# Kernel tuning notes

Measured on AMD Instinct MI355X. Metric: run time of the kernel, lower is better.

## Reference

```python
import jax, jax.numpy as jnp
import numpy as np

B, IN, H, NH = 8192, 1024, 2048, 4
HD = H // NH
EPS = 1e-5


def setup_inputs() -> dict:
    key = jax.random.key(0)
    ks = jax.random.split(key, 8)
    s = 0.02
    return {
        "h_prev": jax.random.normal(ks[0], (B, 1, H), jnp.float32),
        "x": jax.random.normal(ks[1], (B, IN), jnp.float32),
        "W_proj": jax.random.normal(ks[2], (H, IN), jnp.float32) * s,
        "b_proj": jnp.zeros((H,), jnp.float32),
        "W_q": jax.random.normal(ks[3], (H, H), jnp.float32) * s,
        "b_q": jnp.zeros((H,), jnp.float32),
        "W_o": jax.random.normal(ks[4], (H, H), jnp.float32) * s,
        "b_o": jnp.zeros((H,), jnp.float32),
        "W_g": jax.random.normal(ks[5], (H, 2 * H), jnp.float32) * s,
        "b_g": jnp.zeros((H,), jnp.float32),
        "gamma": jnp.ones((H,), jnp.float32),
        "beta": jnp.zeros((H,), jnp.float32),
    }


def _layernorm(y, gamma, beta):
    mu = jnp.mean(y, axis=-1, keepdims=True)
    var = jnp.mean(jnp.square(y - mu), axis=-1, keepdims=True)
    return (y - mu) * jax.lax.rsqrt(var + EPS) * gamma + beta


def reference(h_prev, x, W_proj, b_proj, W_q, b_q, W_o, b_o, W_g, b_g, gamma, beta):
    # input projection: [B, IN] -> [B, H]
    x_proj = x @ W_proj.T + b_proj
    x_exp = x_proj[:, None, :]                      # [B, 1, H]
    # 4-element context along seq dim: [B, 4, H]
    context = jnp.concatenate([h_prev, x_exp, h_prev + x_exp, h_prev * x_exp], axis=1)
    # attention with q_len=1, kv_len=4
    q = (h_prev @ W_q.T + b_q).reshape(B, 1, NH, HD).transpose(0, 2, 1, 3)   # [B,NH,1,HD]
    k = context.reshape(B, 4, NH, HD).transpose(0, 2, 1, 3)                   # [B,NH,4,HD]
    scores = jnp.einsum('bhqd,bhkd->bhqk', q, k) / jnp.sqrt(jnp.float32(HD))  # [B,NH,1,4]
    w = jax.nn.softmax(scores, axis=-1)
    attn = jnp.einsum('bhqk,bhkd->bhqd', w, k)                                # v = k
    attn = attn.transpose(0, 2, 1, 3).reshape(B, 1, H)
    attn = attn @ W_o.T + b_o
    attn = jax.nn.gelu(attn, approximate=False)     # torch F.gelu default is exact erf
    gate_in = jnp.concatenate([h_prev, attn], axis=-1)  # [B,1,2H]
    gate = jax.nn.sigmoid(gate_in @ W_g.T + b_g)
    h_cand = _layernorm(attn + h_prev, gamma, beta)
    h_new = gate * h_cand + (1.0 - gate) * h_prev
    return h_new
```

## Files before the change

### kernel.cpp

```cpp
#include <hip/hip_runtime.h>
#include <hip/hip_bf16.h>
#include <math.h>

#define BATCH 8192
#define IN_DIM 1024
#define H_DIM 2048
#define NHEAD 4
#define HEAD_DIM 512
#define EPS_LN 1e-5f

#define BM 256
#define BN 256
#define BKQ 32
#define NBUF 4

typedef __bf16 bf16x8 __attribute__((ext_vector_type(8)));
typedef short s16x8 __attribute__((ext_vector_type(8)));
typedef float f32x4 __attribute__((ext_vector_type(4)));

__device__ __forceinline__ float b2f(short s) {
  union { unsigned u; float f; } v;
  v.u = ((unsigned)(unsigned short)s) << 16;
  return v.f;
}
__device__ __forceinline__ short f2b(float f) {
  union { float f; unsigned u; } v;
  v.f = f;
  unsigned r = v.u + 0x7fffu + ((v.u >> 16) & 1u);
  return (short)(r >> 16);
}

__device__ __forceinline__ void async_ld16(const short* g, const short* l) {
  __builtin_amdgcn_global_load_lds(
      (const __attribute__((address_space(1))) void*)g,
      (__attribute__((address_space(3))) void*)l, 16, 0, 0);
}

__global__ __launch_bounds__(256) void cvt_k(const float* __restrict__ s,
                                             short* __restrict__ d, int n) {
  int i = (blockIdx.x * 256 + threadIdx.x) * 8;
  if (i >= n) return;
  f32x4 a = *(const f32x4*)(s + i);
  f32x4 b = *(const f32x4*)(s + i + 4);
  s16x8 o;
#pragma unroll
  for (int j = 0; j < 4; j++) o[j] = f2b(a[j]);
#pragma unroll
  for (int j = 0; j < 4; j++) o[4 + j] = f2b(b[j]);
  *(s16x8*)(d + i) = o;
}

enum { EPI_BIAS = 0, EPI_GELU = 1, EPI_GATE = 2 };

template <bool DUAL>
__device__ __forceinline__ void stage_tile(
    const short* __restrict__ A, const short* __restrict__ A2,
    const short* __restrict__ W, short* __restrict__ lds, int t, int K,
    int lda, int rowBase, int colBase, int wv, int rsub, int swz) {
  const int k0 = t * BKQ;
  const short* Asrc = A;
  int ak = k0;
  if (DUAL && k0 >= H_DIM) { Asrc = A2; ak = k0 - H_DIM; }
  short* As = lds + (t & (NBUF - 1)) * (BM * BKQ);
  short* Bs = lds + NBUF * BM * BKQ + (t & (NBUF - 1)) * (BN * BKQ);
  const int r0 = wv * 32;
#pragma unroll
  for (int c = 0; c < 2; c++) {
    const int ra = r0 + c * 16 + rsub;
    async_ld16(Asrc + (size_t)(rowBase + ra) * lda + ak + swz,
               As + (r0 + c * 16) * BKQ);
    async_ld16(W + (size_t)(colBase + ra) * K + k0 + swz,
               Bs + (r0 + c * 16) * BKQ);
  }
}

template <int EPI, bool DUAL>
__global__ __launch_bounds__(512, 2) void gemm_bt(
    const short* __restrict__ A, const short* __restrict__ A2,
    const short* __restrict__ W, const float* __restrict__ bias,
    void* __restrict__ Cv, int K, int lda,
    const short* __restrict__ attg, const float* __restrict__ hprev,
    const float* __restrict__ mu, const float* __restrict__ rstd,
    const float* __restrict__ gamma, const float* __restrict__ beta) {
  extern __shared__ __attribute__((aligned(16))) short lds[];
  const int tid = threadIdx.x;
  const int wv = tid >> 6;
  const int lane = tid & 63;
  const int f = blockIdx.y * gridDim.x + blockIdx.x;
  const int ty = f & 7;
  const int tx = f >> 3;
  const int rowBase = tx * BM;
  const int colBase = ty * BN;
  const int wm = wv >> 2;
  const int wn = wv & 3;
  const int fr = lane & 15;
  const int rsub = lane >> 2;
  const int swz = ((lane & 3) ^ ((lane >> 2) & 3)) << 3;
  const int cbt = ((lane >> 4) ^ (lane & 3)) << 3;
  const int NT = K / BKQ;

  f32x4 acc[8][4] = {};

  stage_tile<DUAL>(A, A2, W, lds, 0, K, lda, rowBase, colBase, wv, rsub, swz);
  stage_tile<DUAL>(A, A2, W, lds, 1, K, lda, rowBase, colBase, wv, rsub, swz);
  stage_tile<DUAL>(A, A2, W, lds, 2, K, lda, rowBase, colBase, wv, rsub, swz);
  asm volatile("s_waitcnt vmcnt(8)" ::: "memory");
  __builtin_amdgcn_s_barrier();
  asm volatile("" ::: "memory");

  for (int t = 0; t < NT; ++t) {
    if (t + 3 < NT)
      stage_tile<DUAL>(A, A2, W, lds, t + 3, K, lda, rowBase, colBase, wv,
                       rsub, swz);

    const short* As = lds + (t & (NBUF - 1)) * (BM * BKQ);
    const short* Bs = lds + NBUF * BM * BKQ + (t & (NBUF - 1)) * (BN * BKQ);
    bf16x8 af[8], bfr[4];
    const short* ap = As + (wm * 128 + fr) * BKQ + cbt;
#pragma unroll
    for (int mi = 0; mi < 8; mi++)
      af[mi] = *(const bf16x8*)(ap + mi * (16 * BKQ));
    const short* bp = Bs + (wn * 64 + fr) * BKQ + cbt;
#pragma unroll
    for (int ni = 0; ni < 4; ni++)
      bfr[ni] = *(const bf16x8*)(bp + ni * (16 * BKQ));

    __builtin_amdgcn_s_setprio(1);
#pragma unroll
    for (int mi = 0; mi < 8; mi++)
#pragma unroll
      for (int ni = 0; ni < 4; ni++)
        acc[mi][ni] = __builtin_amdgcn_mfma_f32_16x16x32_bf16(
            af[mi], bfr[ni], acc[mi][ni], 0, 0, 0);
    __builtin_amdgcn_s_setprio(0);

    if (t + 1 < NT) {
      if (t + 3 < NT)
        asm volatile("s_waitcnt vmcnt(8) lgkmcnt(0)" ::: "memory");
      else if (t + 2 < NT)
        asm volatile("s_waitcnt vmcnt(4) lgkmcnt(0)" ::: "memory");
      else
        asm volatile("s_waitcnt vmcnt(0) lgkmcnt(0)" ::: "memory");
      __builtin_amdgcn_s_barrier();
      asm volatile("" ::: "memory");
    }
  }

  const int ocol0 = colBase + wn * 64 + fr;
  const int orow0 = rowBase + wm * 128 + ((lane >> 4) << 2);
#pragma unroll
  for (int mi = 0; mi < 8; mi++) {
#pragma unroll
    for (int ni = 0; ni < 4; ni++) {
      const int col = ocol0 + ni * 16;
      const float bia = bias[col];
#pragma unroll
      for (int r = 0; r < 4; r++) {
        const int row = orow0 + mi * 16 + r;
        float v = acc[mi][ni][r] + bia;
        const size_t idx = (size_t)row * H_DIM + col;
        if (EPI == EPI_BIAS) {
          ((short*)Cv)[idx] = f2b(v);
        } else if (EPI == EPI_GELU) {
          float g = 0.5f * v * (1.0f + erff(v * 0.70710678118654752f));
          ((short*)Cv)[idx] = f2b(g);
        } else {
          float gate = 1.0f / (1.0f + expf(-v));
          float hp = hprev[idx];
          float y = hp + b2f(attg[idx]);
          float hc = (y - mu[row]) * rstd[row] * gamma[col] + beta[col];
          ((float*)Cv)[idx] = gate * hc + (1.0f - gate) * hp;
        }
      }
    }
  }
}

__global__ __launch_bounds__(256) void attn_k(short* __restrict__ qa,
                                              const float* __restrict__ h,
                                              const short* __restrict__ xp) {
  const int lane = threadIdx.x & 63;
  const int pair = blockIdx.x * 4 + (threadIdx.x >> 6);
  const size_t base =
      (size_t)(pair >> 2) * H_DIM + (size_t)(pair & 3) * HEAD_DIM + lane * 8;
  s16x8 qv = *(const s16x8*)(qa + base);
  f32x4 h0 = *(const f32x4*)(h + base);
  f32x4 h1 = *(const f32x4*)(h + base + 4);
  s16x8 xv = *(const s16x8*)(xp + base);
  float hf[8], xf[8];
  float s1 = 0.f, s2 = 0.f, s4 = 0.f;
#pragma unroll
  for (int j = 0; j < 8; j++) {
    float qf = b2f(qv[j]);
    hf[j] = (j < 4) ? h0[j] : h1[j - 4];
    xf[j] = b2f(xv[j]);
    s1 += qf * hf[j];
    s2 += qf * xf[j];
    s4 += qf * hf[j] * xf[j];
  }
#pragma unroll
  for (int off = 32; off > 0; off >>= 1) {
    s1 += __shfl_xor(s1, off, 64);
    s2 += __shfl_xor(s2, off, 64);
    s4 += __shfl_xor(s4, off, 64);
  }
  const float scale = 0.04419417382415922f;
  float t1 = s1 * scale, t2 = s2 * scale, t3 = (s1 + s2) * scale, t4 = s4 * scale;
  float mx = fmaxf(fmaxf(t1, t2), fmaxf(t3, t4));
  float e1 = expf(t1 - mx), e2 = expf(t2 - mx), e3 = expf(t3 - mx), e4 = expf(t4 - mx);
  float inv = 1.0f / (e1 + e2 + e3 + e4);
  float w1 = e1 * inv, w2 = e2 * inv, w3 = e3 * inv, w4 = e4 * inv;
  float ch = w1 + w3, cx = w2 + w3;
  s16x8 o;
#pragma unroll
  for (int j = 0; j < 8; j++)
    o[j] = f2b(ch * hf[j] + cx * xf[j] + w4 * hf[j] * xf[j]);
  *(s16x8*)(qa + base) = o;
}

__global__ __launch_bounds__(256) void rowstats_k(
    const short* __restrict__ attg, const float* __restrict__ h,
    float* __restrict__ mu, float* __restrict__ rstd) {
  __shared__ float sm[8];
  const int row = blockIdx.x;
  const int tid = threadIdx.x;
  const size_t base = (size_t)row * H_DIM + tid * 8;
  s16x8 a = *(const s16x8*)(attg + base);
  f32x4 h0 = *(const f32x4*)(h + base);
  f32x4 h1 = *(const f32x4*)(h + base + 4);
  float s = 0.f, ss = 0.f;
#pragma unroll
  for (int j = 0; j < 8; j++) {
    float y = b2f(a[j]) + ((j < 4) ? h0[j] : h1[j - 4]);
    s += y;
    ss += y * y;
  }
#pragma unroll
  for (int off = 32; off > 0; off >>= 1) {
    s += __shfl_xor(s, off, 64);
    ss += __shfl_xor(ss, off, 64);
  }
  if ((tid & 63) == 0) {
    sm[tid >> 6] = s;
    sm[4 + (tid >> 6)] = ss;
  }
  __syncthreads();
  if (tid == 0) {
    float S = sm[0] + sm[1] + sm[2] + sm[3];
    float SS = sm[4] + sm[5] + sm[6] + sm[7];
    float m = S * (1.0f / H_DIM);
    float var = SS * (1.0f / H_DIM) - m * m;
    mu[row] = m;
    rstd[row] = rsqrtf(fmaxf(var, 0.0f) + EPS_LN);
  }
}

extern "C" void kernel_launch(void* const* d_in, const int* in_sizes, int n_in,
                              void* d_out, int out_size, void* d_ws,
                              size_t ws_size, hipStream_t stream) {
  (void)in_sizes; (void)n_in; (void)out_size; (void)ws_size;
  const float* h_prev = (const float*)d_in[0];
  const float* x      = (const float*)d_in[1];
  const float* W_proj = (const float*)d_in[2];
  const float* b_proj = (const float*)d_in[3];
  const float* W_q    = (const float*)d_in[4];
  const float* b_q    = (const float*)d_in[5];
  const float* W_o    = (const float*)d_in[6];
  const float* b_o    = (const float*)d_in[7];
  const float* W_g    = (const float*)d_in[8];
  const float* b_g    = (const float*)d_in[9];
  const float* gamma  = (const float*)d_in[10];
  const float* beta   = (const float*)d_in[11];
  float* out = (float*)d_out;

  const size_t BH = (size_t)BATCH * H_DIM;
  const size_t BI = (size_t)BATCH * IN_DIM;
  const size_t NWP = (size_t)H_DIM * IN_DIM;
  const size_t NWQ = (size_t)H_DIM * H_DIM;
  const size_t NWG = (size_t)H_DIM * 2 * H_DIM;

  short* h_bf = (short*)d_ws;
  short* x_bf = h_bf + BH;
  short* wp   = x_bf + BI;
  short* wq   = wp + NWP;
  short* wo   = wq + NWQ;
  short* wg   = wo + NWQ;
  short* bufA = wg + NWG;
  short* bufB = bufA + BH;
  float* mu   = (float*)(bufB + BH);
  float* rstd = mu + BATCH;

  dim3 blk(512);
  dim3 grd(BATCH / BM, H_DIM / BN);
  const int SMEM = 2 * NBUF * BM * BKQ * (int)sizeof(short);
  (void)hipFuncSetAttribute((const void*)gemm_bt<EPI_BIAS, false>,
                            hipFuncAttributeMaxDynamicSharedMemorySize, SMEM);
  (void)hipFuncSetAttribute((const void*)gemm_bt<EPI_GELU, false>,
                            hipFuncAttributeMaxDynamicSharedMemorySize, SMEM);
  (void)hipFuncSetAttribute((const void*)gemm_bt<EPI_GATE, true>,
                            hipFuncAttributeMaxDynamicSharedMemorySize, SMEM);

  dim3 cblk(256);
#define CVT(src, dst, n) \
  cvt_k<<<dim3(((n) / 8 + 255) / 256), cblk, 0, stream>>>(src, dst, (int)(n))

  CVT(h_prev, h_bf, BH);
  CVT(x, x_bf, BI);
  CVT(W_proj, wp, NWP);
  CVT(W_q, wq, NWQ);
  CVT(W_o, wo, NWQ);
  CVT(W_g, wg, NWG);
#undef CVT

  gemm_bt<EPI_BIAS, false><<<grd, blk, SMEM, stream>>>(
      x_bf, nullptr, wp, b_proj, bufA, IN_DIM, IN_DIM,
      nullptr, nullptr, nullptr, nullptr, nullptr, nullptr);
  gemm_bt<EPI_BIAS, false><<<grd, blk, SMEM, stream>>>(
      h_bf, nullptr, wq, b_q, bufB, H_DIM, H_DIM,
      nullptr, nullptr, nullptr, nullptr, nullptr, nullptr);
  attn_k<<<dim3(BATCH * NHEAD / 4), cblk, 0, stream>>>(bufB, h_prev, bufA);
  gemm_bt<EPI_GELU, false><<<grd, blk, SMEM, stream>>>(
      bufB, nullptr, wo, b_o, bufA, H_DIM, H_DIM,
      nullptr, nullptr, nullptr, nullptr, nullptr, nullptr);
  rowstats_k<<<dim3(BATCH), cblk, 0, stream>>>(bufA, h_prev, mu, rstd);
  gemm_bt<EPI_GATE, true><<<grd, blk, SMEM, stream>>>(
      h_bf, bufA, wg, b_g, out, 2 * H_DIM, H_DIM,
      bufA, h_prev, mu, rstd, gamma, beta);
}
```

Baseline: 615.4 us.

## Switch GEMM to BK=64 double-buffered pipeline with mid-tile prefetch issue

Replaces the 4-stage BK=32 LDS ring with a 2-stage BK=64 double buffer. Each k-tile is split into two MFMA halves, and the next-next tile's global loads are issued between them after a barrier. Also changes the LDS XOR swizzle to an 8-chunk scheme and drops the grouped block-index remapping in favour of the plain grid order. The aim is fewer barriers per K and better overlap of loads with MFMA work. The cost is a shallower prefetch distance, an extra barrier per tile, and possibly worse L2 locality from the unremapped grid.

```diff
diff --git a/kernel.cpp b/kernel.cpp
--- a/kernel.cpp
+++ b/kernel.cpp
@@ -11,8 +11,7 @@
 
 #define BM 256
 #define BN 256
-#define BKQ 32
-#define NBUF 4
+#define BK64 64
 
 typedef __bf16 bf16x8 __attribute__((ext_vector_type(8)));
 typedef short s16x8 __attribute__((ext_vector_type(8)));
@@ -56,21 +55,20 @@
 __device__ __forceinline__ void stage_tile(
     const short* __restrict__ A, const short* __restrict__ A2,
     const short* __restrict__ W, short* __restrict__ lds, int t, int K,
-    int lda, int rowBase, int colBase, int wv, int rsub, int swz) {
-  const int k0 = t * BKQ;
+    int lda, int rowBase, int colBase, int wv, int srow, int schunk) {
+  const int k0 = t * BK64;
   const short* Asrc = A;
   int ak = k0;
   if (DUAL && k0 >= H_DIM) { Asrc = A2; ak = k0 - H_DIM; }
-  short* As = lds + (t & (NBUF - 1)) * (BM * BKQ);
-  short* Bs = lds + NBUF * BM * BKQ + (t & (NBUF - 1)) * (BN * BKQ);
-  const int r0 = wv * 32;
-#pragma unroll
-  for (int c = 0; c < 2; c++) {
-    const int ra = r0 + c * 16 + rsub;
-    async_ld16(Asrc + (size_t)(rowBase + ra) * lda + ak + swz,
-               As + (r0 + c * 16) * BKQ);
-    async_ld16(W + (size_t)(colBase + ra) * K + k0 + swz,
-               Bs + (r0 + c * 16) * BKQ);
+  short* As = lds + (t & 1) * (BM * BK64);
+  short* Bs = lds + 2 * BM * BK64 + (t & 1) * (BN * BK64);
+#pragma unroll
+  for (int c = 0; c < 4; c++) {
+    const int r = wv * 32 + c * 8;
+    async_ld16(Asrc + (size_t)(rowBase + r + srow) * lda + ak + schunk,
+               As + r * BK64);
+    async_ld16(W + (size_t)(colBase + r + srow) * K + k0 + schunk,
+               Bs + r * BK64);
   }
 }
 
@@ -86,44 +84,41 @@
   const int tid = threadIdx.x;
   const int wv = tid >> 6;
   const int lane = tid & 63;
-  const int f = blockIdx.y * gridDim.x + blockIdx.x;
-  const int ty = f & 7;
-  const int tx = f >> 3;
-  const int rowBase = tx * BM;
-  const int colBase = ty * BN;
+  const int rowBase = blockIdx.x * BM;
+  const int colBase = blockIdx.y * BN;
   const int wm = wv >> 2;
   const int wn = wv & 3;
   const int fr = lane & 15;
-  const int rsub = lane >> 2;
-  const int swz = ((lane & 3) ^ ((lane >> 2) & 3)) << 3;
-  const int cbt = ((lane >> 4) ^ (lane & 3)) << 3;
-  const int NT = K / BKQ;
+  const int g = lane >> 4;
+  const int srow = lane >> 3;
+  const int schunk = ((lane & 7) ^ srow) * 8;
+  const int ce0 = ((g ^ (lane & 7)) * 8);
+  const int ce1 = ce0 ^ 32;
+  const int apOff = (wm * 128 + fr) * BK64;
+  const int bpOff = (wn * 64 + fr) * BK64;
+  const int NT = K / BK64;
 
   f32x4 acc[8][4] = {};
 
-  stage_tile<DUAL>(A, A2, W, lds, 0, K, lda, rowBase, colBase, wv, rsub, swz);
-  stage_tile<DUAL>(A, A2, W, lds, 1, K, lda, rowBase, colBase, wv, rsub, swz);
-  stage_tile<DUAL>(A, A2, W, lds, 2, K, lda, rowBase, colBase, wv, rsub, swz);
+  stage_tile<DUAL>(A, A2, W, lds, 0, K, lda, rowBase, colBase, wv, srow, schunk);
+  stage_tile<DUAL>(A, A2, W, lds, 1, K, lda, rowBase, colBase, wv, srow, schunk);
   asm volatile("s_waitcnt vmcnt(8)" ::: "memory");
   __builtin_amdgcn_s_barrier();
   asm volatile("" ::: "memory");
 
   for (int t = 0; t < NT; ++t) {
-    if (t + 3 < NT)
-      stage_tile<DUAL>(A, A2, W, lds, t + 3, K, lda, rowBase, colBase, wv,
-                       rsub, swz);
-
-    const short* As = lds + (t & (NBUF - 1)) * (BM * BKQ);
-    const short* Bs = lds + NBUF * BM * BKQ + (t & (NBUF - 1)) * (BN * BKQ);
-    bf16x8 af[8], bfr[4];
-    const short* ap = As + (wm * 128 + fr) * BKQ + cbt;
+    const short* As = lds + (t & 1) * (BM * BK64);
+    const short* Bs = lds + 2 * BM * BK64 + (t & 1) * (BN * BK64);
+    const short* ap = As + apOff;
+    const short* bp = Bs + bpOff;
+
+    bf16x8 a0[8], b0[4];
 #pragma unroll
     for (int mi = 0; mi < 8; mi++)
-      af[mi] = *(const bf16x8*)(ap + mi * (16 * BKQ));
-    const short* bp = Bs + (wn * 64 + fr) * BKQ + cbt;
+      a0[mi] = *(const bf16x8*)(ap + mi * (16 * BK64) + ce0);
 #pragma unroll
     for (int ni = 0; ni < 4; ni++)
-      bfr[ni] = *(const bf16x8*)(bp + ni * (16 * BKQ));
+      b0[ni] = *(const bf16x8*)(bp + ni * (16 * BK64) + ce0);
 
     __builtin_amdgcn_s_setprio(1);
 #pragma unroll
@@ -131,23 +126,46 @@
 #pragma unroll
       for (int ni = 0; ni < 4; ni++)
         acc[mi][ni] = __builtin_amdgcn_mfma_f32_16x16x32_bf16(
-            af[mi], bfr[ni], acc[mi][ni], 0, 0, 0);
+            a0[mi], b0[ni], acc[mi][ni], 0, 0, 0);
     __builtin_amdgcn_s_setprio(0);
 
+    bf16x8 a1[8], b1[4];
+#pragma unroll
+    for (int mi = 0; mi < 8; mi++)
+      a1[mi] = *(const bf16x8*)(ap + mi * (16 * BK64) + ce1);
+#pragma unroll
+    for (int ni = 0; ni < 4; ni++)
+      b1[ni] = *(const bf16x8*)(bp + ni * (16 * BK64) + ce1);
+
+    asm volatile("s_waitcnt lgkmcnt(0)" ::: "memory");
+    __builtin_amdgcn_s_barrier();
+    asm volatile("" ::: "memory");
+
+    if (t + 2 < NT)
+      stage_tile<DUAL>(A, A2, W, lds, t + 2, K, lda, rowBase, colBase, wv,
+                       srow, schunk);
+
+    __builtin_amdgcn_s_setprio(1);
+#pragma unroll
+    for (int mi = 0; mi < 8; mi++)
+#pragma unroll
+      for (int ni = 0; ni < 4; ni++)
+        acc[mi][ni] = __builtin_amdgcn_mfma_f32_16x16x32_bf16(
+            a1[mi], b1[ni], acc[mi][ni], 0, 0, 0);
+    __builtin_amdgcn_s_setprio(0);
+
     if (t + 1 < NT) {
-      if (t + 3 < NT)
-        asm volatile("s_waitcnt vmcnt(8) lgkmcnt(0)" ::: "memory");
-      else if (t + 2 < NT)
-        asm volatile("s_waitcnt vmcnt(4) lgkmcnt(0)" ::: "memory");
+      if (t + 2 < NT)
+        asm volatile("s_waitcnt vmcnt(8)" ::: "memory");
       else
-        asm volatile("s_waitcnt vmcnt(0) lgkmcnt(0)" ::: "memory");
+        asm volatile("s_waitcnt vmcnt(0)" ::: "memory");
       __builtin_amdgcn_s_barrier();
       asm volatile("" ::: "memory");
     }
   }
 
   const int ocol0 = colBase + wn * 64 + fr;
-  const int orow0 = rowBase + wm * 128 + ((lane >> 4) << 2);
+  const int orow0 = rowBase + wm * 128 + (g << 2);
 #pragma unroll
   for (int mi = 0; mi < 8; mi++) {
 #pragma unroll
@@ -162,8 +180,8 @@
         if (EPI == EPI_BIAS) {
           ((short*)Cv)[idx] = f2b(v);
         } else if (EPI == EPI_GELU) {
-          float g = 0.5f * v * (1.0f + erff(v * 0.70710678118654752f));
-          ((short*)Cv)[idx] = f2b(g);
+          float gg = 0.5f * v * (1.0f + erff(v * 0.70710678118654752f));
+          ((short*)Cv)[idx] = f2b(gg);
         } else {
           float gate = 1.0f / (1.0f + expf(-v));
           float hp = hprev[idx];
@@ -292,7 +310,7 @@
 
   dim3 blk(512);
   dim3 grd(BATCH / BM, H_DIM / BN);
-  const int SMEM = 2 * NBUF * BM * BKQ * (int)sizeof(short);
+  const int SMEM = 2 * 2 * BM * BK64 * (int)sizeof(short);
   (void)hipFuncSetAttribute((const void*)gemm_bt<EPI_BIAS, false>,
                             hipFuncAttributeMaxDynamicSharedMemorySize, SMEM);
   (void)hipFuncSetAttribute((const void*)gemm_bt<EPI_GELU, false>,
```

Result: slower. 689.3 us (+12.0%).
